# Performance work log

Hardware: AMD Instinct MI355X
Metric: run time of the kernel (lower is better)

The kernel has to match this reference:

```python
import jax, jax.numpy as jnp
import numpy as np

G = 8          # n_games
D_IN = 512     # per-game input dim (equal for all games)
H1 = 1024
H2 = 1024
A = 128        # max_actions
B = 8192       # batch rows


def setup_inputs() -> dict:
    key = jax.random.key(0)
    ks = jax.random.split(key, 9)
    state = jax.random.normal(ks[0], (B, D_IN), dtype=jnp.float32)
    idx = jax.random.randint(ks[1], (B,), 0, G, dtype=jnp.int32)
    # per-game input linears: uniform(-1/sqrt(fan_in), 1/sqrt(fan_in))
    lim1 = 1.0 / np.sqrt(D_IN)
    W1 = jax.random.uniform(ks[2], (G, D_IN, H1), minval=-lim1, maxval=lim1, dtype=jnp.float32)
    b1 = jax.random.uniform(ks[3], (G, H1), minval=-lim1, maxval=lim1, dtype=jnp.float32)
    # shared linear
    lim2 = 1.0 / np.sqrt(H1)
    W2 = jax.random.uniform(ks[4], (H1, H2), minval=-lim2, maxval=lim2, dtype=jnp.float32)
    b2 = jax.random.uniform(ks[5], (H2,), minval=-lim2, maxval=lim2, dtype=jnp.float32)
    # per-game output heads: uniform(-0.003, 0.003)
    W3 = jax.random.uniform(ks[6], (G, H2, A), minval=-0.003, maxval=0.003, dtype=jnp.float32)
    b3 = jax.random.uniform(ks[7], (G, A), minval=-0.003, maxval=0.003, dtype=jnp.float32)
    return {"state": state, "idx": idx, "W1": W1, "b1": b1, "W2": W2, "b2": b2, "W3": W3, "b3": b3}


def reference(state, idx, W1, b1, W2, b2, W3, b3):
    # Torch code concatenates per-game groups in sorted-unique-idx order,
    # i.e. a stable permutation of rows by idx; reproduce exactly.
    perm = jnp.argsort(idx, stable=True)          # [B]
    s = state[perm]                               # [B, D_IN]
    g = idx[perm]                                 # [B] game of each permuted row
    # routed first layer: compute all games then gather per-row game
    h1_all = jnp.einsum('bd,gdh->bgh', s, W1) + b1            # [B, G, H1]
    h1 = jax.nn.relu(jnp.take_along_axis(h1_all, g[:, None, None], axis=1)[:, 0, :])  # [B, H1]
    h_f = jax.nn.relu(h1 @ W2 + b2)                            # [B, H2]
    a = jnp.tanh(jnp.einsum('bh,gha->bga', h_f, W3) + b3)      # [B, G, A]
    # NOTE: original gathers heads with the ORIGINAL (unpermuted) idx,
    # even though rows of `a` are in permuted order. Reproduce faithfully.
    out = jnp.take_along_axis(a, idx[:, None, None], axis=1)[:, 0, :]  # [B, A]
    return out
```

## Files before the change

### kernel.cpp

```cpp
#include <hip/hip_runtime.h>
#include <math.h>

#define G_GAMES 8
#define D_IN 512
#define H1 1024
#define H2 1024
#define A_DIM 128
#define B_ROWS 8192

typedef short bf16x8 __attribute__((ext_vector_type(8)));
typedef float f32x4 __attribute__((ext_vector_type(4)));

#define WS_OFF   0u
#define WS_PERM  256u
#define WS_SPERM 33280u
#define WS_W1T   (WS_SPERM + B_ROWS*D_IN*2u)
#define WS_W2T   (WS_W1T + G_GAMES*D_IN*H1*2u)
#define WS_W3T   (WS_W2T + (unsigned)H1*H2*2u)
#define WS_H1    (WS_W3T + G_GAMES*H2*A_DIM*2u)
#define WS_HF    WS_SPERM

__device__ __forceinline__ unsigned short f2bf(float x) {
  union { float f; unsigned int u; } v; v.f = x;
  unsigned int r = v.u + 0x7fffu + ((v.u >> 16) & 1u);
  return (unsigned short)(r >> 16);
}

__device__ __forceinline__ void async_load16(const void* gptr, void* ldsptr) {
  __builtin_amdgcn_global_load_lds(
      (const __attribute__((address_space(1))) unsigned int*)gptr,
      (__attribute__((address_space(3))) unsigned int*)ldsptr,
      16, 0, 0);
}

__device__ void sort_256(const int* __restrict__ idx, int* __restrict__ perm,
                         int* __restrict__ off) {
  __shared__ int wtot[4][9];
  __shared__ int wbase[4][9];
  __shared__ int offs[9];
  const int t = threadIdx.x, lane = t & 63, wave = t >> 6;
  int my[32];
#pragma unroll
  for (int i = 0; i < 8; ++i) {
    const int4 a = *(const int4*)(idx + t * 32 + i * 4);
    my[i*4+0] = a.x; my[i*4+1] = a.y; my[i*4+2] = a.z; my[i*4+3] = a.w;
  }
  int local[8] = {0,0,0,0,0,0,0,0};
#pragma unroll
  for (int i = 0; i < 32; ++i) local[my[i]]++;
  int incl[8];
#pragma unroll
  for (int g = 0; g < 8; ++g) {
    int v = local[g];
#pragma unroll
    for (int d = 1; d < 64; d <<= 1) {
      const int n = __shfl_up(v, d);
      if (lane >= d) v += n;
    }
    incl[g] = v;
  }
  if (lane == 63) {
#pragma unroll
    for (int g = 0; g < 8; ++g) wtot[wave][g] = incl[g];
  }
  __syncthreads();
  if (t < 8) {
    int s = 0;
#pragma unroll
    for (int w = 0; w < 4; ++w) { wbase[w][t] = s; s += wtot[w][t]; }
    wtot[0][t] = s;
  }
  __syncthreads();
  if (t == 0) {
    int s = 0;
#pragma unroll
    for (int g = 0; g < 8; ++g) { offs[g] = s; off[g] = s; s += wtot[0][g]; }
    offs[8] = s; off[8] = s;
  }
  __syncthreads();
  int start[8];
#pragma unroll
  for (int g = 0; g < 8; ++g)
    start[g] = offs[g] + wbase[wave][g] + (incl[g] - local[g]);
#pragma unroll
  for (int i = 0; i < 32; ++i) {
    const int g = my[i];
    perm[start[g]++] = t * 32 + i;
  }
}

__device__ void trans_tile(const float* __restrict__ in,
                           unsigned short* __restrict__ out,
                           int R, int C, int xt, int yt, int z) {
  in  += (size_t)z * R * C;
  out += (size_t)z * R * C;
  __shared__ float tile[64][65];
  const int c0 = xt * 64, r0 = yt * 64;
  const int tx = threadIdx.x & 63, ty = threadIdx.x >> 6;
#pragma unroll
  for (int rr = ty; rr < 64; rr += 4)
    tile[rr][tx] = in[(size_t)(r0 + rr) * C + c0 + tx];
  __syncthreads();
#pragma unroll
  for (int cc = ty; cc < 64; cc += 4)
    out[(size_t)(c0 + cc) * R + r0 + tx] = f2bf(tile[tx][cc]);
}

__global__ __launch_bounds__(256) void k_pre1(const float* __restrict__ W1,
                                              const float* __restrict__ W2,
                                              const float* __restrict__ W3,
                                              const int* __restrict__ idx,
                                              unsigned short* __restrict__ W1T,
                                              unsigned short* __restrict__ W2T,
                                              unsigned short* __restrict__ W3T,
                                              int* __restrict__ perm,
                                              int* __restrict__ off) {
  const int b = blockIdx.x;
  if (b < 1024) {
    const int z = b >> 7, r = b & 127;
    trans_tile(W1, W1T, D_IN, H1, r & 15, r >> 4, z);
  } else if (b < 1280) {
    const int r = b - 1024;
    trans_tile(W2, W2T, H1, H2, r & 15, r >> 4, 0);
  } else if (b < 1536) {
    const int r = (b - 1280) & 31, z = (b - 1280) >> 5;
    trans_tile(W3, W3T, H2, A_DIM, r & 1, r >> 1, z);
  } else {
    sort_256(idx, perm, off);
  }
}

__global__ __launch_bounds__(256) void k_gather(const float* __restrict__ state,
                                                const int* __restrict__ perm,
                                                unsigned short* __restrict__ sPerm) {
  const int p = blockIdx.x * 2 + (threadIdx.x >> 7);
  const int c = (threadIdx.x & 127) << 2;
  const int src = perm[p];
  const float4 v = *(const float4*)(state + (size_t)src * D_IN + c);
  ushort4 o;
  o.x = f2bf(v.x); o.y = f2bf(v.y); o.z = f2bf(v.z); o.w = f2bf(v.w);
  *(ushort4*)(sPerm + (size_t)p * D_IN + c) = o;
}

template <int KTOT>
__device__ __forceinline__ void gemm_db8(const unsigned short* const* aP,
                                         const unsigned short* const* bP,
                                         char* smem, int tid, f32x4 acc[4][2]) {
  const int lane = tid & 63, wave = tid >> 6;
  const int wm = wave & 1, wn = wave >> 1;
  const int sw = lane & 15, quad = lane >> 4;
  const int mA = wm * 64 + sw;
  const int nB = wn * 32 + sw;
  char* A0 = smem;          char* A1 = smem + 16384;
  char* B0 = smem + 32768;  char* B1 = smem + 49152;
  const int NIT = KTOT >> 6;
#pragma unroll
  for (int c = 0; c < 2; ++c) {
    async_load16(aP[c], A0 + (wave * 16 + c * 8) * 128);
    async_load16(bP[c], B0 + (wave * 16 + c * 8) * 128);
  }
#pragma unroll 2
  for (int k = 0; k < NIT; ++k) {
    __syncthreads();
    char* A = (k & 1) ? A1 : A0;
    char* B = (k & 1) ? B1 : B0;
    if (k + 1 < NIT) {
      char* An = (k & 1) ? A0 : A1;
      char* Bn = (k & 1) ? B0 : B1;
      const int koff = (k + 1) << 6;
#pragma unroll
      for (int c = 0; c < 2; ++c) {
        async_load16(aP[c] + koff, An + (wave * 16 + c * 8) * 128);
        async_load16(bP[c] + koff, Bn + (wave * 16 + c * 8) * 128);
      }
    }
#pragma unroll
    for (int ks = 0; ks < 2; ++ks) {
      const int u = ((((ks << 2) + quad) ^ (sw & 7)) << 4);
      bf16x8 aF[4], bF[2];
#pragma unroll
      for (int i = 0; i < 4; ++i)
        aF[i] = *(const bf16x8*)(A + (mA + i * 16) * 128 + u);
#pragma unroll
      for (int j = 0; j < 2; ++j)
        bF[j] = *(const bf16x8*)(B + (nB + j * 16) * 128 + u);
#pragma unroll
      for (int i = 0; i < 4; ++i)
#pragma unroll
        for (int j = 0; j < 2; ++j)
          acc[i][j] = __builtin_amdgcn_mfma_f32_16x16x32_bf16(aF[i], bF[j], acc[i][j], 0, 0, 0);
    }
  }
}

__device__ __forceinline__ bool seg_map(const int* __restrict__ off, int T,
                                        int& g, int& seg1, int& row0) {
  int base = 0;
  for (int gg = 0; gg < 8; ++gg) {
    const int s = off[gg], e = off[gg + 1];
    const int nt = (e - s + 127) >> 7;
    if (T < base + nt) { g = gg; seg1 = e; row0 = s + (T - base) * 128; return true; }
    base += nt;
  }
  return false;
}

__device__ __forceinline__ bool seg_map32(const int* __restrict__ off, int T,
                                          int& g, int& seg1, int& row0) {
  int base = 0;
  for (int gg = 0; gg < 8; ++gg) {
    const int s = off[gg], e = off[gg + 1];
    const int nt = (e - s + 31) >> 5;
    if (T < base + nt) { g = gg; seg1 = e; row0 = s + (T - base) * 32; return true; }
    base += nt;
  }
  return false;
}

__device__ __forceinline__ void epi_bf16_512(char* smem, const f32x4 acc[4][2],
                                             const float* bj, int tid,
                                             unsigned short* __restrict__ outp,
                                             size_t ldOut, int row0, int col0,
                                             int vrows) {
  const int lane = tid & 63, wave = tid >> 6;
  const int wm = wave & 1, wn = wave >> 1;
  const int sw = lane & 15, quad = lane >> 4;
  __syncthreads();
#pragma unroll
  for (int i = 0; i < 4; ++i)
#pragma unroll
    for (int j = 0; j < 2; ++j)
#pragma unroll
      for (int r = 0; r < 4; ++r) {
        const int row = wm * 64 + i * 16 + quad * 4 + r;
        const int col = wn * 32 + j * 16 + sw;
        const float v = fmaxf(acc[i][j][r] + bj[j], 0.0f);
        *(unsigned short*)(smem + row * 264 + col * 2) = f2bf(v);
      }
  __syncthreads();
#pragma unroll
  for (int q = 0; q < 4; ++q) {
    const int idxq = q * 512 + tid;
    const int row = idxq >> 4, ch = idxq & 15;
    if (row < vrows) {
      const uint2 lo = *(const uint2*)(smem + row * 264 + ch * 16);
      const uint2 hi = *(const uint2*)(smem + row * 264 + ch * 16 + 8);
      uint4 v; v.x = lo.x; v.y = lo.y; v.z = hi.x; v.w = hi.y;
      *(uint4*)((char*)outp + ((size_t)(row0 + row) * ldOut + col0 + ch * 8) * 2) = v;
    }
  }
}

__global__ __launch_bounds__(512, 4) void k_gemm1(const unsigned short* __restrict__ sPerm,
                                                  const unsigned short* __restrict__ W1T,
                                                  const float* __restrict__ b1,
                                                  const int* __restrict__ off,
                                                  unsigned short* __restrict__ h1out) {
  __shared__ char smem[65536];
  int g, seg1, row0;
  if (!seg_map(off, blockIdx.x, g, seg1, row0)) return;
  const int col0 = blockIdx.y * 128;
  const int tid = threadIdx.x, lane = tid & 63, wave = tid >> 6;
  const int gcol = ((lane & 7) ^ (lane >> 3)) << 3;
  const unsigned short* aP[2];
  const unsigned short* bP[2];
#pragma unroll
  for (int c = 0; c < 2; ++c) {
    const int rl = wave * 16 + c * 8 + (lane >> 3);
    int p = row0 + rl;
    if (p > seg1 - 1) p = seg1 - 1;
    aP[c] = sPerm + (size_t)p * D_IN + gcol;
    bP[c] = W1T + (size_t)g * H1 * D_IN + (size_t)(col0 + rl) * D_IN + gcol;
  }
  f32x4 acc[4][2] = {};
  gemm_db8<D_IN>(aP, bP, smem, tid, acc);
  const int wn = wave >> 1, sw = lane & 15;
  const float* bg = b1 + g * H1;
  float bj[2];
#pragma unroll
  for (int j = 0; j < 2; ++j) bj[j] = bg[col0 + wn * 32 + j * 16 + sw];
  const int vrows = min(128, seg1 - row0);
  epi_bf16_512(smem, acc, bj, tid, h1out, H1, row0, col0, vrows);
}

__global__ __launch_bounds__(512, 4) void k_gemm2(const unsigned short* __restrict__ h1in,
                                                  const unsigned short* __restrict__ W2T,
                                                  const float* __restrict__ b2,
                                                  unsigned short* __restrict__ hfout) {
  __shared__ char smem[65536];
  const int row0 = blockIdx.x * 128, col0 = blockIdx.y * 128;
  const int tid = threadIdx.x, lane = tid & 63, wave = tid >> 6;
  const int gcol = ((lane & 7) ^ (lane >> 3)) << 3;
  const unsigned short* aP[2];
  const unsigned short* bP[2];
#pragma unroll
  for (int c = 0; c < 2; ++c) {
    const int rl = wave * 16 + c * 8 + (lane >> 3);
    aP[c] = h1in + (size_t)(row0 + rl) * H1 + gcol;
    bP[c] = W2T + (size_t)(col0 + rl) * H1 + gcol;
  }
  f32x4 acc[4][2] = {};
  gemm_db8<H1>(aP, bP, smem, tid, acc);
  const int wn = wave >> 1, sw = lane & 15;
  float bj[2];
#pragma unroll
  for (int j = 0; j < 2; ++j) bj[j] = b2[col0 + wn * 32 + j * 16 + sw];
  epi_bf16_512(smem, acc, bj, tid, hfout, H2, row0, col0, 128);
}

__global__ __launch_bounds__(256) void k_gemm3(const unsigned short* __restrict__ hf,
                                               const unsigned short* __restrict__ W3T,
                                               const float* __restrict__ b3,
                                               const int* __restrict__ off,
                                               const int* __restrict__ perm,
                                               float* __restrict__ outp) {
  __shared__ char smem[40960];
  int g, seg1, row0;
  if (!seg_map32(off, blockIdx.x, g, seg1, row0)) return;
  const int tid = threadIdx.x, lane = tid & 63, wave = tid >> 6;
  const int wm = wave & 1, wn = wave >> 1;
  const int sw = lane & 15, quad = lane >> 4;
  const int gcol = ((lane & 7) ^ (lane >> 3)) << 3;
  int q0 = row0 + wave * 8 + (lane >> 3);
  if (q0 > seg1 - 1) q0 = seg1 - 1;
  const unsigned short* aP = hf + (size_t)perm[q0] * H2 + gcol;
  const unsigned short* bP[4];
#pragma unroll
  for (int c = 0; c < 4; ++c) {
    const int rl = wave * 32 + c * 8 + (lane >> 3);
    bP[c] = W3T + (size_t)g * A_DIM * H2 + (size_t)rl * H2 + gcol;
  }
  char* A0 = smem;         char* A1 = smem + 4096;
  char* B0 = smem + 8192;  char* B1 = smem + 24576;
  const int mA = wm * 16 + sw;
  const int nB = wn * 64 + sw;
  f32x4 acc[4] = {};
  async_load16(aP, A0 + (wave * 8) * 128);
#pragma unroll
  for (int c = 0; c < 4; ++c)
    async_load16(bP[c], B0 + (wave * 32 + c * 8) * 128);
#pragma unroll 2
  for (int k = 0; k < (H2 >> 6); ++k) {
    __syncthreads();
    char* A = (k & 1) ? A1 : A0;
    char* B = (k & 1) ? B1 : B0;
    if (k + 1 < (H2 >> 6)) {
      char* An = (k & 1) ? A0 : A1;
      char* Bn = (k & 1) ? B0 : B1;
      const int koff = (k + 1) << 6;
      async_load16(aP + koff, An + (wave * 8) * 128);
#pragma unroll
      for (int c = 0; c < 4; ++c)
        async_load16(bP[c] + koff, Bn + (wave * 32 + c * 8) * 128);
    }
#pragma unroll
    for (int ks = 0; ks < 2; ++ks) {
      const int u = ((((ks << 2) + quad) ^ (sw & 7)) << 4);
      const bf16x8 aF = *(const bf16x8*)(A + mA * 128 + u);
      bf16x8 bF[4];
#pragma unroll
      for (int j = 0; j < 4; ++j)
        bF[j] = *(const bf16x8*)(B + (nB + j * 16) * 128 + u);
#pragma unroll
      for (int j = 0; j < 4; ++j)
        acc[j] = __builtin_amdgcn_mfma_f32_16x16x32_bf16(aF, bF[j], acc[j], 0, 0, 0);
    }
  }
  const float* bg = b3 + g * A_DIM;
  float bj[4];
#pragma unroll
  for (int j = 0; j < 4; ++j) bj[j] = bg[wn * 64 + j * 16 + sw];
  __syncthreads();
#pragma unroll
  for (int j = 0; j < 4; ++j)
#pragma unroll
    for (int r = 0; r < 4; ++r) {
      const int row = wm * 16 + quad * 4 + r;
      const int col = wn * 64 + j * 16 + sw;
      *(float*)(smem + row * 528 + col * 4) = tanhf(acc[j][r] + bj[j]);
    }
  __syncthreads();
#pragma unroll
  for (int qq = 0; qq < 4; ++qq) {
    const int idxq = qq * 256 + tid;
    const int row = idxq >> 5, ch = idxq & 31;
    if (row0 + row < seg1) {
      const uint4 v = *(const uint4*)(smem + row * 528 + ch * 16);
      *(uint4*)((char*)outp + ((size_t)perm[row0 + row] * A_DIM + ch * 4) * 4) = v;
    }
  }
}

extern "C" void kernel_launch(void* const* d_in, const int* in_sizes, int n_in,
                              void* d_out, int out_size, void* d_ws, size_t ws_size,
                              hipStream_t stream) {
  (void)in_sizes; (void)n_in; (void)out_size; (void)ws_size;
  const float* state = (const float*)d_in[0];
  const int*   idx   = (const int*)d_in[1];
  const float* W1    = (const float*)d_in[2];
  const float* b1    = (const float*)d_in[3];
  const float* W2    = (const float*)d_in[4];
  const float* b2    = (const float*)d_in[5];
  const float* W3    = (const float*)d_in[6];
  const float* b3    = (const float*)d_in[7];
  float* outp = (float*)d_out;
  char* ws = (char*)d_ws;
  int* off  = (int*)(ws + WS_OFF);
  int* perm = (int*)(ws + WS_PERM);
  unsigned short* sPerm = (unsigned short*)(ws + WS_SPERM);
  unsigned short* W1T   = (unsigned short*)(ws + WS_W1T);
  unsigned short* W2T   = (unsigned short*)(ws + WS_W2T);
  unsigned short* W3T   = (unsigned short*)(ws + WS_W3T);
  unsigned short* h1    = (unsigned short*)(ws + WS_H1);
  unsigned short* hf    = (unsigned short*)(ws + WS_HF);

  hipLaunchKernelGGL(k_pre1, dim3(1537), dim3(256), 0, stream,
                     W1, W2, W3, idx, W1T, W2T, W3T, perm, off);
  hipLaunchKernelGGL(k_gather, dim3(B_ROWS / 2), dim3(256), 0, stream, state, perm, sPerm);
  hipLaunchKernelGGL(k_gemm1, dim3(72, 8), dim3(512), 0, stream, sPerm, W1T, b1, off, h1);
  hipLaunchKernelGGL(k_gemm2, dim3(64, 8), dim3(512), 0, stream, h1, W2T, b2, hf);
  hipLaunchKernelGGL(k_gemm3, dim3(264), dim3(256), 0, stream, hf, W3T, b3, off, perm, outp);
}
```

Measured before the change: 155.9 us.

## Shrink GEMM1/GEMM2 tiles to 128x64 with 4 waves and XCD-aware block mapping

The first two GEMMs move from 128x128 tiles with 8 waves (512 threads) to 128x64 tiles with 4 waves (256 threads). That doubles the block count, cuts LDS use per block to 48KB, and makes each wave load 4 A chunks and 2 B chunks per K step. GEMM2 also moves from a 2D grid to a 1D grid whose block index is remapped so each XCD owns a contiguous group of row tiles, improving L2 reuse of h1 rows. The goal is better occupancy and load balance across CUs. The cost is more redundant A-tile traffic, since each A tile is now read for 16 column tiles instead of 8.

```diff
diff --git a/kernel.cpp b/kernel.cpp
--- a/kernel.cpp
+++ b/kernel.cpp
@@ -143,22 +143,23 @@
 }
 
 template <int KTOT>
-__device__ __forceinline__ void gemm_db8(const unsigned short* const* aP,
-                                         const unsigned short* const* bP,
-                                         char* smem, int tid, f32x4 acc[4][2]) {
+__device__ __forceinline__ void gemm_db64(const unsigned short* const* aP,
+                                          const unsigned short* const* bP,
+                                          char* smem, int tid, f32x4 acc[4][2]) {
   const int lane = tid & 63, wave = tid >> 6;
   const int wm = wave & 1, wn = wave >> 1;
   const int sw = lane & 15, quad = lane >> 4;
   const int mA = wm * 64 + sw;
   const int nB = wn * 32 + sw;
   char* A0 = smem;          char* A1 = smem + 16384;
-  char* B0 = smem + 32768;  char* B1 = smem + 49152;
+  char* B0 = smem + 32768;  char* B1 = smem + 40960;
   const int NIT = KTOT >> 6;
 #pragma unroll
-  for (int c = 0; c < 2; ++c) {
-    async_load16(aP[c], A0 + (wave * 16 + c * 8) * 128);
+  for (int c = 0; c < 4; ++c)
+    async_load16(aP[c], A0 + (wave * 32 + c * 8) * 128);
+#pragma unroll
+  for (int c = 0; c < 2; ++c)
     async_load16(bP[c], B0 + (wave * 16 + c * 8) * 128);
-  }
 #pragma unroll 2
   for (int k = 0; k < NIT; ++k) {
     __syncthreads();
@@ -169,10 +170,11 @@
       char* Bn = (k & 1) ? B0 : B1;
       const int koff = (k + 1) << 6;
 #pragma unroll
-      for (int c = 0; c < 2; ++c) {
-        async_load16(aP[c] + koff, An + (wave * 16 + c * 8) * 128);
+      for (int c = 0; c < 4; ++c)
+        async_load16(aP[c] + koff, An + (wave * 32 + c * 8) * 128);
+#pragma unroll
+      for (int c = 0; c < 2; ++c)
         async_load16(bP[c] + koff, Bn + (wave * 16 + c * 8) * 128);
-      }
     }
 #pragma unroll
     for (int ks = 0; ks < 2; ++ks) {
@@ -217,11 +219,11 @@
   return false;
 }
 
-__device__ __forceinline__ void epi_bf16_512(char* smem, const f32x4 acc[4][2],
-                                             const float* bj, int tid,
-                                             unsigned short* __restrict__ outp,
-                                             size_t ldOut, int row0, int col0,
-                                             int vrows) {
+__device__ __forceinline__ void epilogue64(char* smem, const f32x4 acc[4][2],
+                                           const float* bj, int tid,
+                                           unsigned short* __restrict__ outp,
+                                           size_t ldOut, int row0, int col0,
+                                           int vrows) {
   const int lane = tid & 63, wave = tid >> 6;
   const int wm = wave & 1, wn = wave >> 1;
   const int sw = lane & 15, quad = lane >> 4;
@@ -235,77 +237,88 @@
         const int row = wm * 64 + i * 16 + quad * 4 + r;
         const int col = wn * 32 + j * 16 + sw;
         const float v = fmaxf(acc[i][j][r] + bj[j], 0.0f);
-        *(unsigned short*)(smem + row * 264 + col * 2) = f2bf(v);
+        *(unsigned short*)(smem + row * 136 + col * 2) = f2bf(v);
       }
   __syncthreads();
 #pragma unroll
   for (int q = 0; q < 4; ++q) {
-    const int idxq = q * 512 + tid;
-    const int row = idxq >> 4, ch = idxq & 15;
+    const int idxq = q * 256 + tid;
+    const int row = idxq >> 3, ch = idxq & 7;
     if (row < vrows) {
-      const uint2 lo = *(const uint2*)(smem + row * 264 + ch * 16);
-      const uint2 hi = *(const uint2*)(smem + row * 264 + ch * 16 + 8);
+      const uint2 lo = *(const uint2*)(smem + row * 136 + ch * 16);
+      const uint2 hi = *(const uint2*)(smem + row * 136 + ch * 16 + 8);
       uint4 v; v.x = lo.x; v.y = lo.y; v.z = hi.x; v.w = hi.y;
       *(uint4*)((char*)outp + ((size_t)(row0 + row) * ldOut + col0 + ch * 8) * 2) = v;
     }
   }
 }
 
-__global__ __launch_bounds__(512, 4) void k_gemm1(const unsigned short* __restrict__ sPerm,
-                                                  const unsigned short* __restrict__ W1T,
-                                                  const float* __restrict__ b1,
-                                                  const int* __restrict__ off,
-                                                  unsigned short* __restrict__ h1out) {
-  __shared__ char smem[65536];
+__global__ __launch_bounds__(256) void k_gemm1(const unsigned short* __restrict__ sPerm,
+                                               const unsigned short* __restrict__ W1T,
+                                               const float* __restrict__ b1,
+                                               const int* __restrict__ off,
+                                               unsigned short* __restrict__ h1out) {
+  __shared__ char smem[49152];
   int g, seg1, row0;
   if (!seg_map(off, blockIdx.x, g, seg1, row0)) return;
-  const int col0 = blockIdx.y * 128;
+  const int col0 = blockIdx.y * 64;
   const int tid = threadIdx.x, lane = tid & 63, wave = tid >> 6;
   const int gcol = ((lane & 7) ^ (lane >> 3)) << 3;
-  const unsigned short* aP[2];
+  const unsigned short* aP[4];
   const unsigned short* bP[2];
 #pragma unroll
-  for (int c = 0; c < 2; ++c) {
-    const int rl = wave * 16 + c * 8 + (lane >> 3);
+  for (int c = 0; c < 4; ++c) {
+    const int rl = wave * 32 + c * 8 + (lane >> 3);
     int p = row0 + rl;
     if (p > seg1 - 1) p = seg1 - 1;
     aP[c] = sPerm + (size_t)p * D_IN + gcol;
+  }
+#pragma unroll
+  for (int c = 0; c < 2; ++c) {
+    const int rl = wave * 16 + c * 8 + (lane >> 3);
     bP[c] = W1T + (size_t)g * H1 * D_IN + (size_t)(col0 + rl) * D_IN + gcol;
   }
   f32x4 acc[4][2] = {};
-  gemm_db8<D_IN>(aP, bP, smem, tid, acc);
+  gemm_db64<D_IN>(aP, bP, smem, tid, acc);
   const int wn = wave >> 1, sw = lane & 15;
   const float* bg = b1 + g * H1;
   float bj[2];
 #pragma unroll
   for (int j = 0; j < 2; ++j) bj[j] = bg[col0 + wn * 32 + j * 16 + sw];
   const int vrows = min(128, seg1 - row0);
-  epi_bf16_512(smem, acc, bj, tid, h1out, H1, row0, col0, vrows);
-}
-
-__global__ __launch_bounds__(512, 4) void k_gemm2(const unsigned short* __restrict__ h1in,
-                                                  const unsigned short* __restrict__ W2T,
-                                                  const float* __restrict__ b2,
-                                                  unsigned short* __restrict__ hfout) {
-  __shared__ char smem[65536];
-  const int row0 = blockIdx.x * 128, col0 = blockIdx.y * 128;
+  epilogue64(smem, acc, bj, tid, h1out, H1, row0, col0, vrows);
+}
+
+__global__ __launch_bounds__(256) void k_gemm2(const unsigned short* __restrict__ h1in,
+                                               const unsigned short* __restrict__ W2T,
+                                               const float* __restrict__ b2,
+                                               unsigned short* __restrict__ hfout) {
+  __shared__ char smem[49152];
+  const int bid = blockIdx.x;
+  const int xcd = bid & 7, s = bid >> 3;
+  const int row0 = (xcd * 8 + (s & 7)) * 128;
+  const int col0 = (s >> 3) * 64;
   const int tid = threadIdx.x, lane = tid & 63, wave = tid >> 6;
   const int gcol = ((lane & 7) ^ (lane >> 3)) << 3;
-  const unsigned short* aP[2];
+  const unsigned short* aP[4];
   const unsigned short* bP[2];
+#pragma unroll
+  for (int c = 0; c < 4; ++c) {
+    const int rl = wave * 32 + c * 8 + (lane >> 3);
+    aP[c] = h1in + (size_t)(row0 + rl) * H1 + gcol;
+  }
 #pragma unroll
   for (int c = 0; c < 2; ++c) {
     const int rl = wave * 16 + c * 8 + (lane >> 3);
-    aP[c] = h1in + (size_t)(row0 + rl) * H1 + gcol;
     bP[c] = W2T + (size_t)(col0 + rl) * H1 + gcol;
   }
   f32x4 acc[4][2] = {};
-  gemm_db8<H1>(aP, bP, smem, tid, acc);
+  gemm_db64<H1>(aP, bP, smem, tid, acc);
   const int wn = wave >> 1, sw = lane & 15;
   float bj[2];
 #pragma unroll
   for (int j = 0; j < 2; ++j) bj[j] = b2[col0 + wn * 32 + j * 16 + sw];
-  epi_bf16_512(smem, acc, bj, tid, hfout, H2, row0, col0, 128);
+  epilogue64(smem, acc, bj, tid, hfout, H2, row0, col0, 128);
 }
 
 __global__ __launch_bounds__(256) void k_gemm3(const unsigned short* __restrict__ hf,
@@ -417,7 +430,7 @@
   hipLaunchKernelGGL(k_pre1, dim3(1537), dim3(256), 0, stream,
                      W1, W2, W3, idx, W1T, W2T, W3T, perm, off);
   hipLaunchKernelGGL(k_gather, dim3(B_ROWS / 2), dim3(256), 0, stream, state, perm, sPerm);
-  hipLaunchKernelGGL(k_gemm1, dim3(72, 8), dim3(512), 0, stream, sPerm, W1T, b1, off, h1);
-  hipLaunchKernelGGL(k_gemm2, dim3(64, 8), dim3(512), 0, stream, h1, W2T, b2, hf);
+  hipLaunchKernelGGL(k_gemm1, dim3(72, 16), dim3(256), 0, stream, sPerm, W1T, b1, off, h1);
+  hipLaunchKernelGGL(k_gemm2, dim3(1024), dim3(256), 0, stream, h1, W2T, b2, hf);
   hipLaunchKernelGGL(k_gemm3, dim3(264), dim3(256), 0, stream, hf, W3T, b3, off, perm, outp);
 }
```

Measured after the change: 156.7 us. Within noise of the previous version (+0.5%).
